# Optimization experiments

Measured on AMD Instinct MI355X. Metric: run time of the kernel, lower is better.

The kernel has to match this reference:

```python
import jax, jax.numpy as jnp
import numpy as np

# --- static config (matches init_kwargs) ---
C = 384        # channels
H = 8          # num_heads
HD = C // H    # head_dim = 48
K = 1024       # patch_size (window)
BASE = 100.0   # rope_freq
MAX_POS = 4096
GRID_SIZE = 0.02
LN_EPS = 1e-5


def _interleave8(x, y, z):
    """Morton-interleave the low 8 bits of x,y,z -> 24-bit code (int32)."""
    key = jnp.zeros_like(x)
    for i in range(8):
        m = 1 << i
        key = key | ((x & m) << (2 * i + 2)) | ((y & m) << (2 * i + 1)) | ((z & m) << (2 * i))
    return key


def _serialize_points(xyz):
    """xyz: (B,3,N) -> (order (B,N) int32, grid (B,N,3) int32). Z-order sort."""
    pts = jnp.transpose(xyz, (0, 2, 1))                       # (B,N,3)
    grid = ((pts - pts.min(axis=1, keepdims=True)) / GRID_SIZE).astype(jnp.int32)
    grid = jnp.clip(grid, 0, 65535)
    gx, gy, gz = grid[..., 0], grid[..., 1], grid[..., 2]
    lo = _interleave8(gx & 255, gy & 255, gz & 255)           # low 24 bits of Morton code
    hi = _interleave8((gx >> 8) & 255, (gy >> 8) & 255, (gz >> 8) & 255)  # high word
    # 48-bit Morton order == lexsort with hi as primary key, lo secondary
    order = jax.vmap(lambda l, h: jnp.lexsort((l, h)))(lo, hi)
    return order.astype(jnp.int32), grid


def _rope_tables(d):
    inv_freq = 1.0 / (BASE ** (jnp.arange(0, d, 2, dtype=jnp.float32) / d))
    t = jnp.arange(MAX_POS, dtype=jnp.float32)
    freqs = t[:, None] * inv_freq[None, :]                    # (MAX_POS, d/2)
    freqs = jnp.concatenate([freqs, freqs], axis=-1)          # (MAX_POS, d)
    return jnp.cos(freqs), jnp.sin(freqs)


def _rotate_half(x):
    h = x.shape[-1] // 2
    return jnp.concatenate([-x[..., h:], x[..., :h]], axis=-1)


def _point_rope(tok, pos):
    """tok: (B,H,N,D) with D%3==0; pos: (B,N,3) int grid coords."""
    D = tok.shape[-1]
    d = D // 3
    pos = jnp.clip(pos, 0, MAX_POS - 1)
    cos, sin = _rope_tables(d)
    outs = []
    for axis, ch in enumerate(jnp.split(tok, 3, axis=-1)):
        p = pos[:, :, axis]                                   # (B,N)
        c = cos[p][:, None]                                   # (B,1,N,d)
        s = sin[p][:, None]
        outs.append(ch * c + _rotate_half(ch) * s)
    return jnp.concatenate(outs, axis=-1)


def _layernorm(x, g, b):
    mu = x.mean(axis=-1, keepdims=True)
    var = ((x - mu) ** 2).mean(axis=-1, keepdims=True)
    return (x - mu) * jax.lax.rsqrt(var + LN_EPS) * g + b


def _forward(x, xyz, ln1_g, ln1_b, qkv_w, qkv_b, proj_w, proj_b,
             ln2_g, ln2_b, ffn_w1, ffn_b1, ffn_w2, ffn_b2):
    B, C_, N = x.shape
    order, grid = _serialize_points(xyz)
    x_sorted = jnp.take_along_axis(x, order[:, None, :], axis=2)          # (B,C,N)
    grid_sorted = jnp.take_along_axis(grid, order[:, :, None], axis=1)    # (B,N,3)
    x_t = jnp.transpose(x_sorted, (0, 2, 1))                              # (B,N,C)
    shortcut = x_t
    xn = _layernorm(x_t, ln1_g, ln1_b)
    pad = (K - N % K) % K
    if pad > 0:
        xn = jnp.pad(xn, ((0, 0), (0, pad), (0, 0)))
        grid_sorted = jnp.pad(grid_sorted, ((0, 0), (0, pad), (0, 0)))
    Np = xn.shape[1]
    nw = Np // K
    qkv = (xn @ qkv_w + qkv_b).reshape(B, Np, 3, H, HD)
    q = jnp.transpose(qkv[:, :, 0], (0, 2, 1, 3))                         # (B,H,Np,HD)
    k = jnp.transpose(qkv[:, :, 1], (0, 2, 1, 3))
    v = jnp.transpose(qkv[:, :, 2], (0, 2, 1, 3))
    q = _point_rope(q, grid_sorted)
    k = _point_rope(k, grid_sorted)
    qw = q.reshape(B, H, nw, K, HD)
    kw = k.reshape(B, H, nw, K, HD)
    vw = v.reshape(B, H, nw, K, HD)
    scale = 1.0 / np.sqrt(HD).astype(np.float32)
    scores = jnp.einsum('bhwqd,bhwkd->bhwqk', qw, kw) * scale             # (B,H,nw,K,K)
    attn = jax.nn.softmax(scores, axis=-1)
    out = jnp.einsum('bhwqk,bhwkd->bhwqd', attn, vw)                      # (B,H,nw,K,HD)
    out = jnp.transpose(out, (0, 2, 3, 1, 4)).reshape(B, Np, C)
    out = out[:, :N]
    out = out @ proj_w + proj_b
    x_t = shortcut + out
    x_t = x_t + (jax.nn.gelu(_layernorm(x_t, ln2_g, ln2_b) @ ffn_w1 + ffn_b1,
                             approximate=False) @ ffn_w2 + ffn_b2)
    x_out = jnp.transpose(x_t, (0, 2, 1))                                 # (B,C,N)
    inv_order = jnp.argsort(order, axis=1)
    x_out = jnp.take_along_axis(x_out, inv_order[:, None, :], axis=2)
    return x_out


def setup_inputs() -> dict:
    key = jax.random.key(0)
    ks = jax.random.split(key, 12)
    B, N = 1, 16384
    s = 0.02
    return {
        'x': jax.random.normal(ks[0], (B, C, N), dtype=jnp.float32),
        'xyz': jax.random.uniform(ks[1], (B, 3, N), dtype=jnp.float32),
        'ln1_g': jnp.ones((C,), jnp.float32),
        'ln1_b': jnp.zeros((C,), jnp.float32),
        'qkv_w': jax.random.normal(ks[2], (C, 3 * C), jnp.float32) * s,
        'qkv_b': jnp.zeros((3 * C,), jnp.float32),
        'proj_w': jax.random.normal(ks[3], (C, C), jnp.float32) * s,
        'proj_b': jnp.zeros((C,), jnp.float32),
        'ln2_g': jnp.ones((C,), jnp.float32),
        'ln2_b': jnp.zeros((C,), jnp.float32),
        'ffn_w1': jax.random.normal(ks[4], (C, 4 * C), jnp.float32) * s,
        'ffn_b1': jnp.zeros((4 * C,), jnp.float32),
        'ffn_w2': jax.random.normal(ks[5], (4 * C, C), jnp.float32) * s,
        'ffn_b2': jnp.zeros((C,), jnp.float32),
    }


def reference(x, xyz, ln1_g, ln1_b, qkv_w, qkv_b, proj_w, proj_b,
              ln2_g, ln2_b, ffn_w1, ffn_b1, ffn_w2, ffn_b2):
    return _forward(x, xyz, ln1_g, ln1_b, qkv_w, qkv_b, proj_w, proj_b,
                    ln2_g, ln2_b, ffn_w1, ffn_b1, ffn_w2, ffn_b2)
```

## Files before the change

### kernel.cpp

```cpp
#include <hip/hip_runtime.h>
#include <hip/hip_bf16.h>

typedef unsigned short u16;
typedef unsigned int u32;
typedef unsigned long long u64;
typedef __attribute__((ext_vector_type(8))) short s16x8;
typedef __attribute__((ext_vector_type(4))) short s16x4;
typedef __attribute__((ext_vector_type(8))) unsigned short u16x8;
typedef __attribute__((ext_vector_type(4))) unsigned short u16x4;
typedef __attribute__((ext_vector_type(4))) float fx4;
typedef __attribute__((ext_vector_type(4))) unsigned int ux4;
typedef __attribute__((ext_vector_type(2))) unsigned int ux2;

__device__ __forceinline__ float bf2f(u16 u){ u32 x=((u32)u)<<16; return __builtin_bit_cast(float,x); }
__device__ __forceinline__ u16 f2bf(float f){ u32 x=__builtin_bit_cast(u32,f); return (u16)((x + 0x7FFFu + ((x>>16)&1u))>>16); }
__device__ __forceinline__ u32 cvtpk(float lo, float hi){
  u32 r; asm("v_cvt_pk_bf16_f32 %0, %1, %2" : "=v"(r) : "v"(lo), "v"(hi)); return r;
}

__device__ __forceinline__ s16x8 ld_bf8(const u16* p){
  s16x4 lo = *(const s16x4*)p;
  s16x4 hi = *(const s16x4*)(p+4);
  s16x8 r;
  r[0]=lo[0]; r[1]=lo[1]; r[2]=lo[2]; r[3]=lo[3];
  r[4]=hi[0]; r[5]=hi[1]; r[6]=hi[2]; r[7]=hi[3];
  return r;
}

__device__ __forceinline__ void gload16(const void* g, void* l){
  __builtin_amdgcn_global_load_lds((__attribute__((address_space(1))) void*)g,
                                   (__attribute__((address_space(3))) void*)l, 16, 0, 0);
}

__device__ __forceinline__ u64 spread3(u32 v){
  u64 x = v & 0xFFFFull;
  x = (x | (x<<32)) & 0x001f00000000ffffull;
  x = (x | (x<<16)) & 0x001f0000ff0000ffull;
  x = (x | (x<<8))  & 0x100f00f00f00f00full;
  x = (x | (x<<4))  & 0x10c30c30c30c30c3ull;
  x = (x | (x<<2))  & 0x1249249249249249ull;
  return x;
}

__global__ __launch_bounds__(256) void min3_kernel(const float* __restrict__ xyz, u32* __restrict__ mins, int N)
{
  int i = blockIdx.x*256 + threadIdx.x;
  float v0 = xyz[i], v1 = xyz[N+i], v2 = xyz[2*N+i];
  #pragma unroll
  for (int s=1;s<64;s<<=1){
    v0 = fminf(v0, __shfl_xor(v0,s));
    v1 = fminf(v1, __shfl_xor(v1,s));
    v2 = fminf(v2, __shfl_xor(v2,s));
  }
  if ((threadIdx.x & 63) == 0){
    atomicMin(mins+0, __builtin_bit_cast(u32, v0));
    atomicMin(mins+1, __builtin_bit_cast(u32, v1));
    atomicMin(mins+2, __builtin_bit_cast(u32, v2));
  }
}

__global__ __launch_bounds__(256) void keys_grid_kernel(const float* __restrict__ xyz, const u32* __restrict__ mins,
        u64* __restrict__ keys, int* __restrict__ gridO, int N)
{
  int i = blockIdx.x*256 + threadIdx.x;
  float mx0 = __builtin_bit_cast(float, mins[0]);
  float mx1 = __builtin_bit_cast(float, mins[1]);
  float mx2 = __builtin_bit_cast(float, mins[2]);
  int gx=(int)((xyz[i]-mx0)/0.02f);     gx = gx<0?0:(gx>65535?65535:gx);
  int gy=(int)((xyz[N+i]-mx1)/0.02f);   gy = gy<0?0:(gy>65535?65535:gy);
  int gz=(int)((xyz[2*N+i]-mx2)/0.02f); gz = gz<0?0:(gz>65535?65535:gz);
  gridO[i*3+0]=gx; gridO[i*3+1]=gy; gridO[i*3+2]=gz;
  u64 mort = (spread3((u32)gx)<<2)|(spread3((u32)gy)<<1)|spread3((u32)gz);
  keys[i] = (mort<<14) | (u64)i;
}

__global__ __launch_bounds__(1024) void bsort_kernel(u64* __restrict__ keys)
{
  __shared__ u64 sk[2048];
  int t = threadIdx.x;
  u64* base = keys + (size_t)blockIdx.x*2048;
  sk[t] = base[t]; sk[t+1024] = base[t+1024];
  for (int size=2; size<=2048; size<<=1){
    for (int stride=size>>1; stride>0; stride>>=1){
      __syncthreads();
      int i = 2*t - (t & (stride-1));
      int j = i + stride;
      u64 a = sk[i], b = sk[j];
      bool up = ((i & size) == 0);
      if ((a > b) == up){ sk[i]=b; sk[j]=a; }
    }
  }
  __syncthreads();
  base[t] = sk[t]; base[t+1024] = sk[t+1024];
}

template<bool FINAL>
__global__ __launch_bounds__(256) void merge_kernel(const u64* __restrict__ src, u64* __restrict__ dst,
        int* __restrict__ order, int L, int N)
{
  int gt = blockIdx.x*256 + threadIdx.x;
  int d0 = gt*8;
  if (d0 >= N) return;
  int pair = d0 / (2*L);
  int base = pair*2*L;
  int ld = d0 - base;
  const u64* A = src + base;
  const u64* B = A + L;
  int lo = ld > L ? ld - L : 0;
  int hi = ld < L ? ld : L;
  while (lo < hi){
    int mid = (lo+hi)>>1;
    if (A[mid] <= B[ld-1-mid]) lo = mid+1; else hi = mid;
  }
  int i = lo, j = ld - lo;
  u64* out = dst + base + ld;
  int* oout = order + base + ld;
  u64 a = (i < L) ? A[i] : ~0ull;
  u64 b = (j < L) ? B[j] : ~0ull;
  #pragma unroll
  for (int e=0;e<8;e++){
    u64 v;
    if (a <= b){ v = a; i++; a = (i<L)?A[i]:~0ull; }
    else       { v = b; j++; b = (j<L)?B[j]:~0ull; }
    out[e] = v;
    if (FINAL) oout[e] = (int)(v & 16383ull);
  }
}

__global__ __launch_bounds__(256) void wtrans4_kernel(const float* __restrict__ qkv_w, const float* __restrict__ proj_w,
    const float* __restrict__ w1, const float* __restrict__ w2,
    u16* __restrict__ qkv_wT, u16* __restrict__ proj_wT, u16* __restrict__ w1T, u16* __restrict__ w2T)
{
  __shared__ float tl[32][33];
  int bid = blockIdx.x;
  const float* W; u16* Wt; int K, Nc, lb;
  if (bid < 432)      { W=qkv_w;  Wt=qkv_wT;  K=384;  Nc=1152; lb=bid; }
  else if (bid < 576) { W=proj_w; Wt=proj_wT; K=384;  Nc=384;  lb=bid-432; }
  else if (bid < 1152){ W=w1;     Wt=w1T;     K=384;  Nc=1536; lb=bid-576; }
  else                { W=w2;     Wt=w2T;     K=1536; Nc=384;  lb=bid-1152; }
  int nb = Nc/32;
  int n0 = (lb % nb)*32;
  int k0 = (lb / nb)*32;
  int t=threadIdx.x; int r=t>>5, c=t&31;
  #pragma unroll
  for (int p=0;p<4;p++) tl[p*8+r][c] = W[(size_t)(k0+p*8+r)*Nc + n0+c];
  __syncthreads();
  #pragma unroll
  for (int p=0;p<4;p++) Wt[(size_t)(n0+p*8+r)*K + k0+c] = f2bf(tl[c][p*8+r]);
}

template<bool BF16IN>
__global__ __launch_bounds__(256) void ln32_kernel(const void* __restrict__ xin, const float* __restrict__ g,
     const float* __restrict__ b, u16* __restrict__ xn, int N)
{
  extern __shared__ char dsm[];
  float* tile = (float*)dsm;
  int n0 = blockIdx.x*32;
  int t = threadIdx.x;
  int tok32 = t&31, cg2 = t>>5;
  #pragma unroll 8
  for (int p=0;p<48;p++){
    int cc = p*8 + cg2;
    float v;
    if (BF16IN) v = bf2f(((const u16*)xin)[(size_t)cc*N + n0 + tok32]);
    else        v = ((const float*)xin)[(size_t)cc*N + n0 + tok32];
    tile[tok32*388 + cc] = v;
  }
  __syncthreads();
  int tok = t>>3, part = t&7;
  const float* row = tile + tok*388 + part*48;
  float s=0.f;
  #pragma unroll
  for (int j=0;j<48;j++) s += row[j];
  s += __shfl_xor(s,1); s += __shfl_xor(s,2); s += __shfl_xor(s,4);
  float mu = s*(1.0f/384.0f);
  float vr=0.f;
  #pragma unroll
  for (int j=0;j<48;j++){ float d=row[j]-mu; vr += d*d; }
  vr += __shfl_xor(vr,1); vr += __shfl_xor(vr,2); vr += __shfl_xor(vr,4);
  float rs = rsqrtf(vr*(1.0f/384.0f) + 1e-5f);
  u16* dst = xn + (size_t)(n0+tok)*384 + part*48;
  #pragma unroll
  for (int q=0;q<6;q++){
    float v[8];
    #pragma unroll
    for (int j=0;j<8;j++){
      int c = part*48 + q*8 + j;
      v[j] = (row[q*8+j]-mu)*rs*g[c] + b[c];
    }
    ux4 o;
    o[0]=cvtpk(v[0],v[1]); o[1]=cvtpk(v[2],v[3]); o[2]=cvtpk(v[4],v[5]); o[3]=cvtpk(v[6],v[7]);
    *(ux4*)(dst + q*8) = o;
  }
}

__device__ __forceinline__ float gelu_f(float v){
  return 0.5f*v*(1.0f + erff(v*0.7071067811865475f));
}

template<int EPI>
__global__ __launch_bounds__(256) void gemm128_kernel(const u16* __restrict__ A, const u16* __restrict__ Bt,
    const float* __restrict__ bias, u16* __restrict__ outB, float* __restrict__ outF,
    const float* __restrict__ resF, const u16* __restrict__ resB, int M, int Nout, int K)
{
  __shared__ u16 Al[128*64];
  __shared__ u16 Bl[128*64];
  int nmt = M>>7;
  int m0 = (blockIdx.x % nmt)<<7;
  int n0 = (blockIdx.x / nmt)<<7;
  int t = threadIdx.x, lane=t&63, wv=t>>6, wr=wv>>1, wc=wv&1;
  int fr = lane&15, fg = lane>>4;
  fx4 acc[4][4];
  #pragma unroll
  for (int i=0;i<4;i++)
  #pragma unroll
  for (int j=0;j<4;j++) acc[i][j]=(fx4){0.f,0.f,0.f,0.f};
  int srow = wv*32 + (lane>>3);
  int swz  = ((lane&7) ^ ((lane>>3)&7)) * 8;
  const u16* ApL = A  + (size_t)(m0+srow)*K + swz;
  const u16* BpL = Bt + (size_t)(n0+srow)*K + swz;
  u16* AlW = Al + wv*2048 + lane*8;
  u16* BlW = Bl + wv*2048 + lane*8;
  const u16* a_base = Al + (wr*64+fr)*64;
  const u16* b_base = Bl + (wc*64+fr)*64;
  int swr = fr & 7;
  for (int k0=0;k0<K;k0+=64){
    #pragma unroll
    for (int i=0;i<4;i++){
      gload16(ApL + k0 + (size_t)i*8*K, AlW + i*512);
      gload16(BpL + k0 + (size_t)i*8*K, BlW + i*512);
    }
    __syncthreads();
    #pragma unroll
    for (int ks=0;ks<2;ks++){
      int soff = (((ks*4+fg) ^ swr) << 3);
      s16x8 a[4], b[4];
      #pragma unroll
      for (int mi=0;mi<4;mi++) a[mi] = *(const s16x8*)(a_base + mi*1024 + soff);
      #pragma unroll
      for (int ni=0;ni<4;ni++) b[ni] = *(const s16x8*)(b_base + ni*1024 + soff);
      #pragma unroll
      for (int mi=0;mi<4;mi++)
      #pragma unroll
      for (int ni=0;ni<4;ni++)
        acc[mi][ni] = __builtin_amdgcn_mfma_f32_16x16x32_bf16(a[mi], b[ni], acc[mi][ni], 0,0,0);
    }
    __syncthreads();
  }
  if (EPI==0 || EPI==1){
    #pragma unroll
    for (int mi=0;mi<4;mi++)
    #pragma unroll
    for (int ni=0;ni<4;ni++){
      int c = n0 + wc*64 + ni*16 + fr;
      float bi = bias[c];
      int mb = m0 + wr*64 + mi*16 + fg*4;
      #pragma unroll
      for (int j=0;j<4;j++){
        float vv = acc[mi][ni][j] + bi;
        if (EPI==1) vv = gelu_f(vv);
        outB[(size_t)(mb+j)*Nout + c] = f2bf(vv);
      }
    }
  } else if (EPI==2){
    #pragma unroll
    for (int mi=0;mi<4;mi++)
    #pragma unroll
    for (int ni=0;ni<4;ni++){
      int c = n0 + wc*64 + ni*16 + fr;
      float bi = bias[c];
      size_t idx = (size_t)c*M + m0 + wr*64 + mi*16 + fg*4;
      fx4 r4 = *(const fx4*)(resF + idx);
      ux2 p;
      p[0] = cvtpk(acc[mi][ni][0]+bi+r4[0], acc[mi][ni][1]+bi+r4[1]);
      p[1] = cvtpk(acc[mi][ni][2]+bi+r4[2], acc[mi][ni][3]+bi+r4[3]);
      *(ux2*)(outB + idx) = p;
    }
  } else {
    #pragma unroll
    for (int mi=0;mi<4;mi++)
    #pragma unroll
    for (int ni=0;ni<4;ni++){
      int c = n0 + wc*64 + ni*16 + fr;
      float bi = bias[c];
      size_t idx = (size_t)c*M + m0 + wr*64 + mi*16 + fg*4;
      ux2 rb = *(const ux2*)(resB + idx);
      fx4 o;
      o[0] = acc[mi][ni][0] + bi + bf2f((u16)rb[0]);
      o[1] = acc[mi][ni][1] + bi + bf2f((u16)(rb[0]>>16));
      o[2] = acc[mi][ni][2] + bi + bf2f((u16)rb[1]);
      o[3] = acc[mi][ni][3] + bi + bf2f((u16)(rb[1]>>16));
      *(fx4*)(outF + idx) = o;
    }
  }
}

#define LOG2_100_O8 0.8304820237218405f

__global__ __launch_bounds__(256) void rope_kernel(const u16* __restrict__ qkv, const int* __restrict__ order,
    const int* __restrict__ gridO, u16* __restrict__ Qp, u16* __restrict__ Kp, u16* __restrict__ Vp, int N)
{
  __shared__ float csm[64][24][2];
  __shared__ int origs[64];
  int i0 = blockIdx.x<<6;
  int t = threadIdx.x;
  if (t<64) origs[t] = order[i0+t];
  __syncthreads();
  for (int idx=t; idx<64*24; idx+=256){
    int tok = idx/24, slot = idx - tok*24;
    int a = slot>>3, fi = slot&7;
    int pos = gridO[(size_t)origs[tok]*3 + a];
    pos = pos<0?0:(pos>4095?4095:pos);
    float invf = __builtin_amdgcn_exp2f(-(float)fi * LOG2_100_O8);
    float ang = (float)pos * invf;
    csm[tok][slot][0] = __cosf(ang);
    csm[tok][slot][1] = __sinf(ang);
  }
  __syncthreads();
  int tok = t&63;
  int i = i0 + tok;
  const u16* src = qkv + (size_t)origs[tok]*1152;
  for (int h=t>>6; h<8; h+=4){
    size_t dst = ((size_t)h*N + i)*48;
    #pragma unroll
    for (int a=0;a<3;a++){
      u16x8 qa = *(const u16x8*)(src + h*48 + a*16);
      u16x8 qb = *(const u16x8*)(src + h*48 + a*16 + 8);
      u16x8 ka = *(const u16x8*)(src + 384 + h*48 + a*16);
      u16x8 kb = *(const u16x8*)(src + 384 + h*48 + a*16 + 8);
      float oqa[8], oqb[8], oka[8], okb[8];
      #pragma unroll
      for (int j=0;j<8;j++){
        float c0 = csm[tok][a*8+j][0], s0 = csm[tok][a*8+j][1];
        float ql = bf2f(qa[j]), qh = bf2f(qb[j]);
        float kl = bf2f(ka[j]), kh = bf2f(kb[j]);
        oqa[j] = ql*c0 - qh*s0;
        oqb[j] = qh*c0 + ql*s0;
        oka[j] = kl*c0 - kh*s0;
        okb[j] = kh*c0 + kl*s0;
      }
      ux4 OQa, OQb, OKa, OKb;
      #pragma unroll
      for (int p=0;p<4;p++){
        OQa[p]=cvtpk(oqa[2*p],oqa[2*p+1]);
        OQb[p]=cvtpk(oqb[2*p],oqb[2*p+1]);
        OKa[p]=cvtpk(oka[2*p],oka[2*p+1]);
        OKb[p]=cvtpk(okb[2*p],okb[2*p+1]);
      }
      *(ux4*)(Qp + dst + a*16) = OQa;
      *(ux4*)(Qp + dst + a*16 + 8) = OQb;
      *(ux4*)(Kp + dst + a*16) = OKa;
      *(ux4*)(Kp + dst + a*16 + 8) = OKb;
      u16x8 va = *(const u16x8*)(src + 768 + h*48 + a*16);
      u16x8 vb = *(const u16x8*)(src + 768 + h*48 + a*16 + 8);
      *(u16x8*)(Vp + dst + a*16) = va;
      *(u16x8*)(Vp + dst + a*16 + 8) = vb;
    }
  }
}

#define ATTN_SCALE 0.14433756729740643f
#define E2SCALE 0.2082354550504211f
#define DEFER_RAW 55.0f
#define KSTRIDE 68

__global__ __launch_bounds__(512) void attn5_kernel(const u16* __restrict__ Qp, const u16* __restrict__ Kp,
    const u16* __restrict__ Vp, const int* __restrict__ order, u16* __restrict__ attn, int N, int nw)
{
  __shared__ u16 Kl[64*KSTRIDE];
  __shared__ u16 Vl[48*KSTRIDE];
  __shared__ u16 Pl[8][32*KSTRIDE];
  int b = blockIdx.x;
  int hw = b & 127;
  int qc = b >> 7;
  int w = hw % nw, h = hw / nw;
  int t = threadIdx.x, lane = t&63, wv = t>>6;
  int fr = lane & 15, fg = lane >> 4;
  size_t base = ((size_t)h*N + (size_t)w*1024);
  int q0 = qc*256 + wv*32;
  bool kact = t < 384;
  int krow = t/6, kc = t - krow*6;
  const u16* ksrc = Kp + (base + krow)*48 + kc*8;
  u16* kdst = Kl + krow*KSTRIDE + kc*8;
  int s2 = t - 128;
  bool vact = t >= 128;
  int vrow = s2/6, vc = s2 - vrow*6;
  const u16* vsrc = Vp + (base + vrow)*48 + vc*8;
  int vkey = vrow ^ (vc<<3);
  if (t < 256){ ux2 z = {0,0}; *(ux2*)&Kl[(t>>2)*KSTRIDE + 48 + (t&3)*4] = z; }
  s16x8 qf[2][2];
  s16x8 zf = {0,0,0,0,0,0,0,0};
  #pragma unroll
  for (int n=0;n<2;n++){
    const u16* qrow = Qp + (base + q0 + n*16 + fr)*48;
    qf[n][0] = ld_bf8(qrow + fg*8);
    qf[n][1] = (fg < 2) ? ld_bf8(qrow + 32 + fg*8) : zf;
  }

  float m0r = -3.4e38f, m1r = -3.4e38f;
  float ls0 = 0.f, ls1 = 0.f;
  fx4 o00=(fx4){0.f,0.f,0.f,0.f}, o01=o00, o02=o00, o10=o00, o11=o00, o12=o00;
  u16* pl = Pl[wv];
  ux4 kreg = {0,0,0,0}, vreg = {0,0,0,0};
  if (kact) kreg = *(const ux4*)ksrc;
  if (vact) vreg = *(const ux4*)vsrc;

  for (int c=0;c<16;c++){
    __syncthreads();
    if (kact){
      ux2 lo; lo[0]=kreg[0]; lo[1]=kreg[1];
      ux2 hi; hi[0]=kreg[2]; hi[1]=kreg[3];
      *(ux2*)kdst = lo; *(ux2*)(kdst+4) = hi;
    }
    if (vact){
      u16* vcp = Vl + vkey;
      vcp[(vc*8+0)*KSTRIDE] = (u16)vreg[0];
      vcp[(vc*8+1)*KSTRIDE] = (u16)(vreg[0]>>16);
      vcp[(vc*8+2)*KSTRIDE] = (u16)vreg[1];
      vcp[(vc*8+3)*KSTRIDE] = (u16)(vreg[1]>>16);
      vcp[(vc*8+4)*KSTRIDE] = (u16)vreg[2];
      vcp[(vc*8+5)*KSTRIDE] = (u16)(vreg[2]>>16);
      vcp[(vc*8+6)*KSTRIDE] = (u16)vreg[3];
      vcp[(vc*8+7)*KSTRIDE] = (u16)(vreg[3]>>16);
    }
    __syncthreads();
    if (c < 15){
      if (kact) kreg = *(const ux4*)(ksrc + (size_t)(c+1)*3072);
      if (vact) vreg = *(const ux4*)(vsrc + (size_t)(c+1)*3072);
    }
    fx4 s0[4], s1v[4];
    __builtin_amdgcn_s_setprio(1);
    #pragma unroll
    for (int m=0;m<4;m++){
      s0[m]=(fx4){0.f,0.f,0.f,0.f}; s1v[m]=s0[m];
      #pragma unroll
      for (int s=0;s<2;s++){
        s16x8 af = ld_bf8(Kl + (m*16+fr)*KSTRIDE + s*32 + fg*8);
        s0[m]  = __builtin_amdgcn_mfma_f32_16x16x32_bf16(af, qf[0][s], s0[m],  0,0,0);
        s1v[m] = __builtin_amdgcn_mfma_f32_16x16x32_bf16(af, qf[1][s], s1v[m], 0,0,0);
      }
    }
    __builtin_amdgcn_s_setprio(0);
    float pm0 = -3.4e38f, pm1 = -3.4e38f;
    #pragma unroll
    for (int m=0;m<4;m++){
      float a0 = fmaxf(fmaxf(s0[m][0],s0[m][1]), fmaxf(s0[m][2],s0[m][3]));
      float a1 = fmaxf(fmaxf(s1v[m][0],s1v[m][1]), fmaxf(s1v[m][2],s1v[m][3]));
      pm0 = fmaxf(pm0, a0); pm1 = fmaxf(pm1, a1);
    }
    pm0 = fmaxf(pm0, __shfl_xor(pm0,16)); pm0 = fmaxf(pm0, __shfl_xor(pm0,32));
    pm1 = fmaxf(pm1, __shfl_xor(pm1,16)); pm1 = fmaxf(pm1, __shfl_xor(pm1,32));
    if (!__all((pm0 <= m0r + DEFER_RAW) & (pm1 <= m1r + DEFER_RAW))){
      float nm0 = fmaxf(m0r, pm0), nm1 = fmaxf(m1r, pm1);
      float f0 = __builtin_amdgcn_exp2f((m0r - nm0)*E2SCALE);
      float f1 = __builtin_amdgcn_exp2f((m1r - nm1)*E2SCALE);
      ls0 *= f0; ls1 *= f1;
      m0r = nm0; m1r = nm1;
      #pragma unroll
      for (int j=0;j<4;j++){
        float g0 = __shfl(f0, fg*4+j);
        float g1 = __shfl(f1, fg*4+j);
        o00[j]*=g0; o01[j]*=g0; o02[j]*=g0;
        o10[j]*=g1; o11[j]*=g1; o12[j]*=g1;
      }
    }
    #pragma unroll
    for (int m=0;m<4;m++){
      float e0[4], e1[4];
      #pragma unroll
      for (int j=0;j<4;j++){
        e0[j] = __builtin_amdgcn_exp2f((s0[m][j]-m0r)*E2SCALE);
        e1[j] = __builtin_amdgcn_exp2f((s1v[m][j]-m1r)*E2SCALE);
        ls0 += e0[j]; ls1 += e1[j];
      }
      ux2 P0, P1;
      P0[0]=cvtpk(e0[0],e0[1]); P0[1]=cvtpk(e0[2],e0[3]);
      P1[0]=cvtpk(e1[0],e1[1]); P1[1]=cvtpk(e1[2],e1[3]);
      *(ux2*)&pl[(fr)*KSTRIDE + m*16 + fg*4]      = P0;
      *(ux2*)&pl[(16+fr)*KSTRIDE + m*16 + fg*4]   = P1;
    }
    __builtin_amdgcn_s_setprio(1);
    #pragma unroll
    for (int s=0;s<2;s++){
      s16x8 pa0 = ld_bf8(pl + fr*KSTRIDE + s*32 + fg*8);
      s16x8 pa1 = ld_bf8(pl + (16+fr)*KSTRIDE + s*32 + fg*8);
      int kb = s*32 + fg*8;
      s16x8 vb0 = ld_bf8(Vl + (fr)*KSTRIDE    + (kb ^ ((fr)&56)));
      s16x8 vb1 = ld_bf8(Vl + (16+fr)*KSTRIDE + (kb ^ ((16+fr)&56)));
      s16x8 vb2 = ld_bf8(Vl + (32+fr)*KSTRIDE + (kb ^ ((32+fr)&56)));
      o00 = __builtin_amdgcn_mfma_f32_16x16x32_bf16(pa0, vb0, o00, 0,0,0);
      o01 = __builtin_amdgcn_mfma_f32_16x16x32_bf16(pa0, vb1, o01, 0,0,0);
      o02 = __builtin_amdgcn_mfma_f32_16x16x32_bf16(pa0, vb2, o02, 0,0,0);
      o10 = __builtin_amdgcn_mfma_f32_16x16x32_bf16(pa1, vb0, o10, 0,0,0);
      o11 = __builtin_amdgcn_mfma_f32_16x16x32_bf16(pa1, vb1, o11, 0,0,0);
      o12 = __builtin_amdgcn_mfma_f32_16x16x32_bf16(pa1, vb2, o12, 0,0,0);
    }
    __builtin_amdgcn_s_setprio(0);
  }
  ls0 += __shfl_xor(ls0,16); ls0 += __shfl_xor(ls0,32);
  ls1 += __shfl_xor(ls1,16); ls1 += __shfl_xor(ls1,32);
  float r0 = 1.0f/ls0, r1 = 1.0f/ls1;
  const int* ord = order + w*1024 + q0;
  #pragma unroll
  for (int j=0;j<4;j++){
    float inv0 = __shfl(r0, fg*4+j);
    float inv1 = __shfl(r1, fg*4+j);
    int orig0 = ord[fg*4+j];
    u16* dst0 = attn + (size_t)orig0*384 + h*48;
    dst0[fr]      = f2bf(o00[j]*inv0);
    dst0[16+fr]   = f2bf(o01[j]*inv0);
    dst0[32+fr]   = f2bf(o02[j]*inv0);
    int orig1 = ord[16 + fg*4+j];
    u16* dst1 = attn + (size_t)orig1*384 + h*48;
    dst1[fr]      = f2bf(o10[j]*inv1);
    dst1[16+fr]   = f2bf(o11[j]*inv1);
    dst1[32+fr]   = f2bf(o12[j]*inv1);
  }
}

extern "C" void kernel_launch(void* const* d_in, const int* in_sizes, int n_in,
                              void* d_out, int out_size, void* d_ws, size_t ws_size,
                              hipStream_t stream)
{
  (void)n_in; (void)out_size; (void)ws_size;
  const float* x     = (const float*)d_in[0];
  const float* xyz   = (const float*)d_in[1];
  const float* ln1_g = (const float*)d_in[2];
  const float* ln1_b = (const float*)d_in[3];
  const float* qkv_w = (const float*)d_in[4];
  const float* qkv_b = (const float*)d_in[5];
  const float* proj_w= (const float*)d_in[6];
  const float* proj_b= (const float*)d_in[7];
  const float* ln2_g = (const float*)d_in[8];
  const float* ln2_b = (const float*)d_in[9];
  const float* ffn_w1= (const float*)d_in[10];
  const float* ffn_b1= (const float*)d_in[11];
  const float* ffn_w2= (const float*)d_in[12];
  const float* ffn_b2= (const float*)d_in[13];
  int N = in_sizes[0]/384;
  int nw = N/1024;
  char* wsp = (char*)d_ws;
  size_t off = 0;
  auto alloc = [&](size_t bytes)->char*{ char* p = wsp + off; off = (off + bytes + 255) & ~(size_t)255; return p; };
  int*  order   = (int*)alloc((size_t)N*4);
  int*  gridO   = (int*)alloc((size_t)N*12);
  u32*  mins    = (u32*)alloc(256);
  u64*  keysA   = (u64*)alloc((size_t)N*8);
  u64*  keysB   = (u64*)alloc((size_t)N*8);
  u16*  qkv_wT  = (u16*)alloc((size_t)1152*384*2);
  u16*  proj_wT = (u16*)alloc((size_t)384*384*2);
  u16*  w1T     = (u16*)alloc((size_t)1536*384*2);
  u16*  w2T     = (u16*)alloc((size_t)384*1536*2);
  u16*  xn      = (u16*)alloc((size_t)N*384*2);
  u16*  Qp      = (u16*)alloc((size_t)N*48*8*2);
  u16*  Kp      = (u16*)alloc((size_t)N*48*8*2);
  u16*  Vp      = (u16*)alloc((size_t)N*48*8*2);
  u16*  qkvb    = (u16*)alloc((size_t)N*1152*2);
  u16*  y1b     = (u16*)alloc((size_t)N*384*2);
  u16*  attn    = xn;
  u16*  xn2     = qkvb;
  u16*  mid     = xn;
  float* outF = (float*)d_out;

  hipMemsetAsync(mins, 0xFF, 12, stream);
  min3_kernel<<<N/256, 256, 0, stream>>>(xyz, mins, N);
  keys_grid_kernel<<<N/256, 256, 0, stream>>>(xyz, mins, keysA, gridO, N);
  bsort_kernel<<<N/2048, 1024, 0, stream>>>(keysA);
  merge_kernel<false><<<N/2048, 256, 0, stream>>>(keysA, keysB, order, 2048, N);
  merge_kernel<false><<<N/2048, 256, 0, stream>>>(keysB, keysA, order, 4096, N);
  merge_kernel<true><<<N/2048, 256, 0, stream>>>(keysA, keysB, order, 8192, N);

  wtrans4_kernel<<<1728, 256, 0, stream>>>(qkv_w, proj_w, ffn_w1, ffn_w2, qkv_wT, proj_wT, w1T, w2T);
  ln32_kernel<false><<<N/32, 256, 32*388*4, stream>>>(x, ln1_g, ln1_b, xn, N);
  gemm128_kernel<0><<<(N/128)*(1152/128), 256, 0, stream>>>(xn, qkv_wT, qkv_b, qkvb, nullptr, nullptr, nullptr, N, 1152, 384);
  rope_kernel<<<N/64, 256, 0, stream>>>(qkvb, order, gridO, Qp, Kp, Vp, N);
  attn5_kernel<<<8*nw*4, 512, 0, stream>>>(Qp, Kp, Vp, order, attn, N, nw);
  gemm128_kernel<2><<<(N/128)*(384/128), 256, 0, stream>>>(attn, proj_wT, proj_b, y1b, nullptr, x, nullptr, N, 384, 384);
  ln32_kernel<true><<<N/32, 256, 32*388*4, stream>>>(y1b, ln2_g, ln2_b, xn2, N);
  gemm128_kernel<1><<<(N/128)*(1536/128), 256, 0, stream>>>(xn2, w1T, ffn_b1, mid, nullptr, nullptr, nullptr, N, 1536, 384);
  gemm128_kernel<3><<<(N/128)*(384/128), 256, 0, stream>>>(mid, w2T, ffn_b2, nullptr, outF, nullptr, y1b, N, 384, 1536);
}
```

Measured before the change: 291.8 us.

## Double-buffer K/V tiles in attention and compute row sums via MFMA

The attention kernel now keeps two shared-memory K/V buffers. The next chunk is written into the alternate buffer after the PV MFMAs, which cuts the two barriers per iteration down to one. Softmax row sums are no longer accumulated with scalar adds and cross-lane shuffles; an extra MFMA against a vector of ones produces them in the output accumulator layout. This adds shared memory and MFMA work in exchange for less synchronisation and fewer VALU/shuffle ops; the sums now come from bf16-rounded probabilities.

```diff
diff --git a/kernel.cpp b/kernel.cpp
--- a/kernel.cpp
+++ b/kernel.cpp
@@ -364,11 +364,11 @@
 #define DEFER_RAW 55.0f
 #define KSTRIDE 68
 
-__global__ __launch_bounds__(512) void attn5_kernel(const u16* __restrict__ Qp, const u16* __restrict__ Kp,
+__global__ __launch_bounds__(512) void attn7_kernel(const u16* __restrict__ Qp, const u16* __restrict__ Kp,
     const u16* __restrict__ Vp, const int* __restrict__ order, u16* __restrict__ attn, int N, int nw)
 {
-  __shared__ u16 Kl[64*KSTRIDE];
-  __shared__ u16 Vl[48*KSTRIDE];
+  __shared__ u16 Kl[2][64*KSTRIDE];
+  __shared__ u16 Vl[2][48*KSTRIDE];
   __shared__ u16 Pl[8][32*KSTRIDE];
   int b = blockIdx.x;
   int hw = b & 127;
@@ -381,13 +381,17 @@
   bool kact = t < 384;
   int krow = t/6, kc = t - krow*6;
   const u16* ksrc = Kp + (base + krow)*48 + kc*8;
-  u16* kdst = Kl + krow*KSTRIDE + kc*8;
+  int koff = krow*KSTRIDE + kc*8;
   int s2 = t - 128;
   bool vact = t >= 128;
   int vrow = s2/6, vc = s2 - vrow*6;
   const u16* vsrc = Vp + (base + vrow)*48 + vc*8;
   int vkey = vrow ^ (vc<<3);
-  if (t < 256){ ux2 z = {0,0}; *(ux2*)&Kl[(t>>2)*KSTRIDE + 48 + (t&3)*4] = z; }
+  if (t < 256){
+    ux2 z = {0,0};
+    *(ux2*)&Kl[0][(t>>2)*KSTRIDE + 48 + (t&3)*4] = z;
+    *(ux2*)&Kl[1][(t>>2)*KSTRIDE + 48 + (t&3)*4] = z;
+  }
   s16x8 qf[2][2];
   s16x8 zf = {0,0,0,0,0,0,0,0};
   #pragma unroll
@@ -396,34 +400,38 @@
     qf[n][0] = ld_bf8(qrow + fg*8);
     qf[n][1] = (fg < 2) ? ld_bf8(qrow + 32 + fg*8) : zf;
   }
+  s16x8 ones;
+  #pragma unroll
+  for (int j=0;j<8;j++) ones[j] = (short)0x3F80;
 
   float m0r = -3.4e38f, m1r = -3.4e38f;
-  float ls0 = 0.f, ls1 = 0.f;
-  fx4 o00=(fx4){0.f,0.f,0.f,0.f}, o01=o00, o02=o00, o10=o00, o11=o00, o12=o00;
+  fx4 o00=(fx4){0.f,0.f,0.f,0.f}, o01=o00, o02=o00, o03=o00, o10=o00, o11=o00, o12=o00, o13=o00;
   u16* pl = Pl[wv];
   ux4 kreg = {0,0,0,0}, vreg = {0,0,0,0};
   if (kact) kreg = *(const ux4*)ksrc;
   if (vact) vreg = *(const ux4*)vsrc;
+  if (kact){
+    ux2 lo; lo[0]=kreg[0]; lo[1]=kreg[1];
+    ux2 hi; hi[0]=kreg[2]; hi[1]=kreg[3];
+    *(ux2*)(Kl[0]+koff) = lo; *(ux2*)(Kl[0]+koff+4) = hi;
+  }
+  if (vact){
+    u16* vcp = Vl[0] + vkey;
+    vcp[(vc*8+0)*KSTRIDE] = (u16)vreg[0];
+    vcp[(vc*8+1)*KSTRIDE] = (u16)(vreg[0]>>16);
+    vcp[(vc*8+2)*KSTRIDE] = (u16)vreg[1];
+    vcp[(vc*8+3)*KSTRIDE] = (u16)(vreg[1]>>16);
+    vcp[(vc*8+4)*KSTRIDE] = (u16)vreg[2];
+    vcp[(vc*8+5)*KSTRIDE] = (u16)(vreg[2]>>16);
+    vcp[(vc*8+6)*KSTRIDE] = (u16)vreg[3];
+    vcp[(vc*8+7)*KSTRIDE] = (u16)(vreg[3]>>16);
+  }
+  __syncthreads();
 
   for (int c=0;c<16;c++){
-    __syncthreads();
-    if (kact){
-      ux2 lo; lo[0]=kreg[0]; lo[1]=kreg[1];
-      ux2 hi; hi[0]=kreg[2]; hi[1]=kreg[3];
-      *(ux2*)kdst = lo; *(ux2*)(kdst+4) = hi;
-    }
-    if (vact){
-      u16* vcp = Vl + vkey;
-      vcp[(vc*8+0)*KSTRIDE] = (u16)vreg[0];
-      vcp[(vc*8+1)*KSTRIDE] = (u16)(vreg[0]>>16);
-      vcp[(vc*8+2)*KSTRIDE] = (u16)vreg[1];
-      vcp[(vc*8+3)*KSTRIDE] = (u16)(vreg[1]>>16);
-      vcp[(vc*8+4)*KSTRIDE] = (u16)vreg[2];
-      vcp[(vc*8+5)*KSTRIDE] = (u16)(vreg[2]>>16);
-      vcp[(vc*8+6)*KSTRIDE] = (u16)vreg[3];
-      vcp[(vc*8+7)*KSTRIDE] = (u16)(vreg[3]>>16);
-    }
-    __syncthreads();
+    int cur = c & 1;
+    const u16* kl = Kl[cur];
+    const u16* vl = Vl[cur];
     if (c < 15){
       if (kact) kreg = *(const ux4*)(ksrc + (size_t)(c+1)*3072);
       if (vact) vreg = *(const ux4*)(vsrc + (size_t)(c+1)*3072);
@@ -435,7 +443,7 @@
       s0[m]=(fx4){0.f,0.f,0.f,0.f}; s1v[m]=s0[m];
       #pragma unroll
       for (int s=0;s<2;s++){
-        s16x8 af = ld_bf8(Kl + (m*16+fr)*KSTRIDE + s*32 + fg*8);
+        s16x8 af = ld_bf8(kl + (m*16+fr)*KSTRIDE + s*32 + fg*8);
         s0[m]  = __builtin_amdgcn_mfma_f32_16x16x32_bf16(af, qf[0][s], s0[m],  0,0,0);
         s1v[m] = __builtin_amdgcn_mfma_f32_16x16x32_bf16(af, qf[1][s], s1v[m], 0,0,0);
       }
@@ -454,14 +462,13 @@
       float nm0 = fmaxf(m0r, pm0), nm1 = fmaxf(m1r, pm1);
       float f0 = __builtin_amdgcn_exp2f((m0r - nm0)*E2SCALE);
       float f1 = __builtin_amdgcn_exp2f((m1r - nm1)*E2SCALE);
-      ls0 *= f0; ls1 *= f1;
       m0r = nm0; m1r = nm1;
       #pragma unroll
       for (int j=0;j<4;j++){
         float g0 = __shfl(f0, fg*4+j);
         float g1 = __shfl(f1, fg*4+j);
-        o00[j]*=g0; o01[j]*=g0; o02[j]*=g0;
-        o10[j]*=g1; o11[j]*=g1; o12[j]*=g1;
+        o00[j]*=g0; o01[j]*=g0; o02[j]*=g0; o03[j]*=g0;
+        o10[j]*=g1; o11[j]*=g1; o12[j]*=g1; o13[j]*=g1;
       }
     }
     #pragma unroll
@@ -471,7 +478,6 @@
       for (int j=0;j<4;j++){
         e0[j] = __builtin_amdgcn_exp2f((s0[m][j]-m0r)*E2SCALE);
         e1[j] = __builtin_amdgcn_exp2f((s1v[m][j]-m1r)*E2SCALE);
-        ls0 += e0[j]; ls1 += e1[j];
       }
       ux2 P0, P1;
       P0[0]=cvtpk(e0[0],e0[1]); P0[1]=cvtpk(e0[2],e0[3]);
@@ -482,29 +488,49 @@
     __builtin_amdgcn_s_setprio(1);
     #pragma unroll
     for (int s=0;s<2;s++){
-      s16x8 pa0 = ld_bf8(pl + fr*KSTRIDE + s*32 + fg*8);
-      s16x8 pa1 = ld_bf8(pl + (16+fr)*KSTRIDE + s*32 + fg*8);
       int kb = s*32 + fg*8;
-      s16x8 vb0 = ld_bf8(Vl + (fr)*KSTRIDE    + (kb ^ ((fr)&56)));
-      s16x8 vb1 = ld_bf8(Vl + (16+fr)*KSTRIDE + (kb ^ ((16+fr)&56)));
-      s16x8 vb2 = ld_bf8(Vl + (32+fr)*KSTRIDE + (kb ^ ((32+fr)&56)));
+      s16x8 pa0 = ld_bf8(pl + fr*KSTRIDE + kb);
+      s16x8 pa1 = ld_bf8(pl + (16+fr)*KSTRIDE + kb);
+      s16x8 vb0 = ld_bf8(vl + (fr)*KSTRIDE    + (kb ^ ((fr)&56)));
+      s16x8 vb1 = ld_bf8(vl + (16+fr)*KSTRIDE + (kb ^ ((16+fr)&56)));
+      s16x8 vb2 = ld_bf8(vl + (32+fr)*KSTRIDE + (kb ^ ((32+fr)&56)));
       o00 = __builtin_amdgcn_mfma_f32_16x16x32_bf16(pa0, vb0, o00, 0,0,0);
       o01 = __builtin_amdgcn_mfma_f32_16x16x32_bf16(pa0, vb1, o01, 0,0,0);
       o02 = __builtin_amdgcn_mfma_f32_16x16x32_bf16(pa0, vb2, o02, 0,0,0);
+      o03 = __builtin_amdgcn_mfma_f32_16x16x32_bf16(pa0, ones, o03, 0,0,0);
       o10 = __builtin_amdgcn_mfma_f32_16x16x32_bf16(pa1, vb0, o10, 0,0,0);
       o11 = __builtin_amdgcn_mfma_f32_16x16x32_bf16(pa1, vb1, o11, 0,0,0);
       o12 = __builtin_amdgcn_mfma_f32_16x16x32_bf16(pa1, vb2, o12, 0,0,0);
+      o13 = __builtin_amdgcn_mfma_f32_16x16x32_bf16(pa1, ones, o13, 0,0,0);
     }
     __builtin_amdgcn_s_setprio(0);
-  }
-  ls0 += __shfl_xor(ls0,16); ls0 += __shfl_xor(ls0,32);
-  ls1 += __shfl_xor(ls1,16); ls1 += __shfl_xor(ls1,32);
-  float r0 = 1.0f/ls0, r1 = 1.0f/ls1;
+    if (c < 15){
+      u16* kln = Kl[cur^1];
+      u16* vln = Vl[cur^1];
+      if (kact){
+        ux2 lo; lo[0]=kreg[0]; lo[1]=kreg[1];
+        ux2 hi; hi[0]=kreg[2]; hi[1]=kreg[3];
+        *(ux2*)(kln+koff) = lo; *(ux2*)(kln+koff+4) = hi;
+      }
+      if (vact){
+        u16* vcp = vln + vkey;
+        vcp[(vc*8+0)*KSTRIDE] = (u16)vreg[0];
+        vcp[(vc*8+1)*KSTRIDE] = (u16)(vreg[0]>>16);
+        vcp[(vc*8+2)*KSTRIDE] = (u16)vreg[1];
+        vcp[(vc*8+3)*KSTRIDE] = (u16)(vreg[1]>>16);
+        vcp[(vc*8+4)*KSTRIDE] = (u16)vreg[2];
+        vcp[(vc*8+5)*KSTRIDE] = (u16)(vreg[2]>>16);
+        vcp[(vc*8+6)*KSTRIDE] = (u16)vreg[3];
+        vcp[(vc*8+7)*KSTRIDE] = (u16)(vreg[3]>>16);
+      }
+      __syncthreads();
+    }
+  }
   const int* ord = order + w*1024 + q0;
   #pragma unroll
   for (int j=0;j<4;j++){
-    float inv0 = __shfl(r0, fg*4+j);
-    float inv1 = __shfl(r1, fg*4+j);
+    float inv0 = 1.0f / o03[j];
+    float inv1 = 1.0f / o13[j];
     int orig0 = ord[fg*4+j];
     u16* dst0 = attn + (size_t)orig0*384 + h*48;
     dst0[fr]      = f2bf(o00[j]*inv0);
@@ -574,7 +600,7 @@
   ln32_kernel<false><<<N/32, 256, 32*388*4, stream>>>(x, ln1_g, ln1_b, xn, N);
   gemm128_kernel<0><<<(N/128)*(1152/128), 256, 0, stream>>>(xn, qkv_wT, qkv_b, qkvb, nullptr, nullptr, nullptr, N, 1152, 384);
   rope_kernel<<<N/64, 256, 0, stream>>>(qkvb, order, gridO, Qp, Kp, Vp, N);
-  attn5_kernel<<<8*nw*4, 512, 0, stream>>>(Qp, Kp, Vp, order, attn, N, nw);
+  attn7_kernel<<<8*nw*4, 512, 0, stream>>>(Qp, Kp, Vp, order, attn, N, nw);
   gemm128_kernel<2><<<(N/128)*(384/128), 256, 0, stream>>>(attn, proj_wT, proj_b, y1b, nullptr, x, nullptr, N, 384, 384);
   ln32_kernel<true><<<N/32, 256, 32*388*4, stream>>>(y1b, ln2_g, ln2_b, xn2, N);
   gemm128_kernel<1><<<(N/128)*(1536/128), 256, 0, stream>>>(xn2, w1T, ffn_b1, mid, nullptr, nullptr, nullptr, N, 1536, 384);
```

After: 291.7 us. Within noise of the previous version (-0.1%).
